# Optimization experiments

Measured on AMD Instinct MI355X. Metric: run time of the kernel, lower is better.

Reference implementation:

```python
import jax, jax.numpy as jnp
import numpy as np

N, C, HR, WR, HS, WS, S = 4, 128, 64, 64, 64, 64, 64


def setup_inputs() -> dict:
    key = jax.random.key(0)
    k1, k2, k3 = jax.random.split(key, 3)
    feat_ref = jax.random.normal(k1, (N, C, HR, WR), dtype=jnp.float32)
    feat_src = jax.random.normal(k2, (N, C, HS, WS), dtype=jnp.float32)
    # sampling locations in unnormalized source-pixel coordinates [0, WS)
    grids = jax.random.uniform(k3, (N, S, 2, HR, WR), dtype=jnp.float32) * WS
    mask = jnp.ones((N, S, HR, WR), dtype=jnp.float32)
    return {"feat_ref": feat_ref, "feat_src": feat_src, "grids": grids, "mask": mask}


def _corr_forward(feat_ref, feat_src, grids, mask):
    n, c, hr, wr = feat_ref.shape
    hs, ws = feat_src.shape[-2:]
    s = grids.shape[1]
    p = hr * wr
    fr = feat_ref.reshape(n, c, p)          # [N,C,P]
    fs = feat_src.reshape(n, c, hs * ws)    # [N,C,HsWs]
    # full pairwise correlation volume (normalize=False path)
    corr = jnp.einsum('ncp,ncq->npq', fr, fs)  # [N,P,HsWs]

    # grids NS2HrWr -> [N,P,2,S]  (matches permute(0,3,4,2,1).reshape)
    g = jnp.transpose(grids, (0, 3, 4, 2, 1)).reshape(n, p, 2, s)
    gx, gy = g[:, :, 0, :], g[:, :, 1, :]   # [N,P,S]

    # torch grid_sample, align_corners=False: normalized->pixel maps to coord-0.5
    ix = gx - 0.5
    iy = gy - 0.5
    x0 = jnp.floor(ix)
    y0 = jnp.floor(iy)
    wx1 = ix - x0
    wy1 = iy - y0
    x0i = x0.astype(jnp.int32)
    y0i = y0.astype(jnp.int32)

    out = jnp.zeros((n, p, s), corr.dtype)
    msum = jnp.zeros((n, p, s), corr.dtype)  # grid_sample of all-ones (zeros padding)
    for dx, wx in ((0, 1.0 - wx1), (1, wx1)):
        for dy, wy in ((0, 1.0 - wy1), (1, wy1)):
            xi = x0i + dx
            yi = y0i + dy
            inb = ((xi >= 0) & (xi < ws) & (yi >= 0) & (yi < hs)).astype(corr.dtype)
            idx = jnp.clip(yi, 0, hs - 1) * ws + jnp.clip(xi, 0, ws - 1)  # [N,P,S]
            val = jnp.take_along_axis(corr, idx, axis=-1)
            w = wx * wy * inb
            out = out + w * val
            msum = msum + w

    # mask[mask < 0.9999] = 0; mask[mask > 0] = 1
    corr_mask = jnp.where(msum < 0.9999, 0.0, 1.0).astype(corr.dtype)
    out = out * corr_mask

    # [N,P,S] -> [N,S,Hr,Wr]
    out = out.reshape(n, hr, wr, s).transpose(0, 3, 1, 2)
    corr_mask = corr_mask.reshape(n, hr, wr, s).transpose(0, 3, 1, 2)

    out = out * mask
    corr_mask = corr_mask * mask
    return out, corr_mask


def reference(feat_ref, feat_src, grids, mask):
    return _corr_forward(feat_ref, feat_src, grids, mask)
```

## Files before the change

kernel.cpp:

```cpp
#include <hip/hip_runtime.h>
#include <hip/hip_fp16.h>
#include <cstdint>
#include <cstddef>

#define NB 4
#define C 128
#define P 4096
#define S 64
#define Q 4096
#define WS_DIM 64
#define HS_DIM 64

#define FS_T_OFF 0

__device__ __forceinline__ void gload_lds16(const void* g, void* l) {
  __builtin_amdgcn_global_load_lds(
      (const __attribute__((address_space(1))) unsigned int*)g,
      (__attribute__((address_space(3))) unsigned int*)l, 16, 0, 0);
}

__global__ __launch_bounds__(256) void transpose_fs_h(
    const float* __restrict__ fs, __half* __restrict__ ws) {
  __shared__ float tile[32][65];
  int b = blockIdx.x;
  int n  = b >> 8;
  int t  = b & 255;
  int rti = t & 3;
  int cti = t >> 2;
  int r0 = rti << 5, c0 = cti << 6;
  const float* Sp = fs + (size_t)n * C * P;
  __half*      Dp = ws + FS_T_OFF + (size_t)n * Q * C;
  int tx = threadIdx.x & 15, ty = threadIdx.x >> 4;
#pragma unroll
  for (int i = 0; i < 2; ++i) {
    int row = ty + 16 * i;
    float4 v = *reinterpret_cast<const float4*>(
        &Sp[(size_t)(r0 + row) * P + c0 + tx * 4]);
    tile[row][tx * 4 + 0] = v.x;
    tile[row][tx * 4 + 1] = v.y;
    tile[row][tx * 4 + 2] = v.z;
    tile[row][tx * 4 + 3] = v.w;
  }
  __syncthreads();
  int ox = threadIdx.x & 7, oy = threadIdx.x >> 3;
#pragma unroll
  for (int i = 0; i < 2; ++i) {
    int prow = oy + 32 * i;
    __half2 h01 = __floats2half2_rn(tile[ox * 4 + 0][prow], tile[ox * 4 + 1][prow]);
    __half2 h23 = __floats2half2_rn(tile[ox * 4 + 2][prow], tile[ox * 4 + 3][prow]);
    uint2 pk;
    pk.x = *reinterpret_cast<unsigned int*>(&h01);
    pk.y = *reinterpret_cast<unsigned int*>(&h23);
    *reinterpret_cast<uint2*>(&Dp[(size_t)(c0 + prow) * C + r0 + ox * 4]) = pk;
  }
}

__global__ __launch_bounds__(256) void corr_main(
    const __half* __restrict__ ws, const float* __restrict__ fr_g,
    const float* __restrict__ grids, const float* __restrict__ mask,
    float* __restrict__ out, float* __restrict__ cmo) {
  const __half* fs_h = ws + FS_T_OFF;

  __shared__ __align__(16) unsigned char stg[4][16384];
  __shared__ int4   s_idx[4][65];
  __shared__ float4 s_w[4][65];
  __shared__ float  s_cmm[4][68];
  __shared__ float  s_out[4][68];
  __shared__ float  fr_lds[4][132];

  int b    = blockIdx.x;
  int xcd  = b & 7;
  int n    = xcd >> 1;
  int half = xcd & 1;
  int grp  = b >> 3;
  int wv   = threadIdx.x >> 6;
  int lane = threadIdx.x & 63;
  int t    = threadIdx.x;
  int p_base = ((half << 9) + grp) << 2;

#pragma unroll
  for (int i = 0; i < 2; ++i) {
    int e  = t + 256 * i;
    int c  = e >> 2;
    int po = e & 3;
    fr_lds[po][c] = fr_g[((size_t)n * C + c) * P + p_base + po];
  }

  {
    int s  = t >> 2;
    int po = t & 3;
    int pp = p_base + po;
    float gx = grids[(((size_t)n * S + s) * 2 + 0) * P + pp];
    float gy = grids[(((size_t)n * S + s) * 2 + 1) * P + pp];
    float mval = mask[((size_t)n * S + s) * P + pp];
    float ix = gx - 0.5f, iy = gy - 0.5f;
    float x0f = floorf(ix), y0f = floorf(iy);
    float wx1 = ix - x0f, wy1 = iy - y0f;
    float wx0 = 1.0f - wx1, wy0 = 1.0f - wy1;
    int x0 = (int)x0f, y0 = (int)y0f;
    int4 idx; float4 w4;
    float msum = 0.0f;
    {
      int xi = x0, yi = y0;
      bool inb = (xi >= 0) & (xi < WS_DIM) & (yi >= 0) & (yi < HS_DIM);
      float wk = inb ? wx0 * wy0 : 0.0f;
      msum += wk;
      idx.x = min(max(yi, 0), HS_DIM - 1) * WS_DIM + min(max(xi, 0), WS_DIM - 1);
      w4.x = wk;
    }
    {
      int xi = x0, yi = y0 + 1;
      bool inb = (xi >= 0) & (xi < WS_DIM) & (yi >= 0) & (yi < HS_DIM);
      float wk = inb ? wx0 * wy1 : 0.0f;
      msum += wk;
      idx.y = min(max(yi, 0), HS_DIM - 1) * WS_DIM + min(max(xi, 0), WS_DIM - 1);
      w4.y = wk;
    }
    {
      int xi = x0 + 1, yi = y0;
      bool inb = (xi >= 0) & (xi < WS_DIM) & (yi >= 0) & (yi < HS_DIM);
      float wk = inb ? wx1 * wy0 : 0.0f;
      msum += wk;
      idx.z = min(max(yi, 0), HS_DIM - 1) * WS_DIM + min(max(xi, 0), WS_DIM - 1);
      w4.z = wk;
    }
    {
      int xi = x0 + 1, yi = y0 + 1;
      bool inb = (xi >= 0) & (xi < WS_DIM) & (yi >= 0) & (yi < HS_DIM);
      float wk = inb ? wx1 * wy1 : 0.0f;
      msum += wk;
      idx.w = min(max(yi, 0), HS_DIM - 1) * WS_DIM + min(max(xi, 0), WS_DIM - 1);
      w4.w = wk;
    }
    float cm  = (msum < 0.9999f) ? 0.0f : 1.0f;
    float cmm = cm * mval;
    s_idx[po][s] = idx;
    s_w[po][s]   = w4;
    s_cmm[po][s] = cmm;
    cmo[((size_t)n * S + s) * P + pp] = cmm;
  }
  __syncthreads();

  int cg = lane & 3;
  int sl = lane >> 2;
  float frv[4][8];
#pragma unroll
  for (int j = 0; j < 4; ++j) {
    float4 a = *reinterpret_cast<const float4*>(&fr_lds[wv][j * 32 + cg * 8]);
    float4 bq = *reinterpret_cast<const float4*>(&fr_lds[wv][j * 32 + cg * 8 + 4]);
    frv[j][0] = a.x; frv[j][1] = a.y; frv[j][2] = a.z; frv[j][3] = a.w;
    frv[j][4] = bq.x; frv[j][5] = bq.y; frv[j][6] = bq.z; frv[j][7] = bq.w;
  }
  const __half* fsb = fs_h + (size_t)n * Q * C + cg * 8;
  unsigned char* mystg = &stg[wv][0];

#pragma unroll 1
  for (int r = 0; r < 4; ++r) {
    int s = r * 16 + sl;
    int4   id4 = s_idx[wv][s];
    float4 w4  = s_w[wv][s];
    float  cms = s_cmm[wv][s];
    const __half* q0 = fsb + (size_t)id4.x * C;
    const __half* q1 = fsb + (size_t)id4.y * C;
    const __half* q2 = fsb + (size_t)id4.z * C;
    const __half* q3 = fsb + (size_t)id4.w * C;

    __builtin_amdgcn_sched_barrier(0);
#pragma unroll
    for (int j = 0; j < 4; ++j) gload_lds16(q0 + j * 32, mystg + (0 * 4 + j) * 1024);
#pragma unroll
    for (int j = 0; j < 4; ++j) gload_lds16(q1 + j * 32, mystg + (1 * 4 + j) * 1024);
#pragma unroll
    for (int j = 0; j < 4; ++j) gload_lds16(q2 + j * 32, mystg + (2 * 4 + j) * 1024);
#pragma unroll
    for (int j = 0; j < 4; ++j) gload_lds16(q3 + j * 32, mystg + (3 * 4 + j) * 1024);

    float d0 = 0.0f, d1 = 0.0f, d2 = 0.0f, d3 = 0.0f;
    asm volatile("s_waitcnt vmcnt(8)" ::: "memory");
#pragma unroll
    for (int j = 0; j < 4; ++j) {
      const __half2* h0 = reinterpret_cast<const __half2*>(mystg + (0 * 4 + j) * 1024 + lane * 16);
      const __half2* h1 = reinterpret_cast<const __half2*>(mystg + (1 * 4 + j) * 1024 + lane * 16);
#pragma unroll
      for (int i = 0; i < 4; ++i) {
        float2 f0 = __half22float2(h0[i]);
        float2 f1 = __half22float2(h1[i]);
        d0 = fmaf(frv[j][2 * i], f0.x, d0);
        d0 = fmaf(frv[j][2 * i + 1], f0.y, d0);
        d1 = fmaf(frv[j][2 * i], f1.x, d1);
        d1 = fmaf(frv[j][2 * i + 1], f1.y, d1);
      }
    }
    asm volatile("s_waitcnt vmcnt(0)" ::: "memory");
#pragma unroll
    for (int j = 0; j < 4; ++j) {
      const __half2* h2 = reinterpret_cast<const __half2*>(mystg + (2 * 4 + j) * 1024 + lane * 16);
      const __half2* h3 = reinterpret_cast<const __half2*>(mystg + (3 * 4 + j) * 1024 + lane * 16);
#pragma unroll
      for (int i = 0; i < 4; ++i) {
        float2 f2 = __half22float2(h2[i]);
        float2 f3 = __half22float2(h3[i]);
        d2 = fmaf(frv[j][2 * i], f2.x, d2);
        d2 = fmaf(frv[j][2 * i + 1], f2.y, d2);
        d3 = fmaf(frv[j][2 * i], f3.x, d3);
        d3 = fmaf(frv[j][2 * i + 1], f3.y, d3);
      }
    }
    float acc = fmaf(w4.x, d0, 0.0f);
    acc = fmaf(w4.y, d1, acc);
    acc = fmaf(w4.z, d2, acc);
    acc = fmaf(w4.w, d3, acc);
    acc += __shfl_xor(acc, 1);
    acc += __shfl_xor(acc, 2);
    if (cg == 0) s_out[wv][s] = acc * cms;
  }
  __syncthreads();
  {
    int s = t >> 2, w2 = t & 3;
    out[((size_t)n * S + s) * P + (p_base + w2)] = s_out[w2][s];
  }
}

extern "C" void kernel_launch(void* const* d_in, const int* in_sizes, int n_in,
                              void* d_out, int out_size, void* d_ws, size_t ws_size,
                              hipStream_t stream) {
  const float* feat_ref = (const float*)d_in[0];
  const float* feat_src = (const float*)d_in[1];
  const float* grids    = (const float*)d_in[2];
  const float* mask     = (const float*)d_in[3];
  __half* ws = (__half*)d_ws;
  float* out = (float*)d_out;
  float* cmo = out + (size_t)NB * S * P;

  transpose_fs_h<<<1024, 256, 0, stream>>>(feat_src, ws);
  corr_main<<<4096, 256, 0, stream>>>(ws, feat_ref, grids, mask, out, cmo);
}
```

Measured before the change: 132.7 us.

## Fetch horizontally adjacent bilinear taps as one contiguous padded row span

Result: slower. 140.4 us (+5.8%).

```diff
diff --git a/kernel.cpp b/kernel.cpp
--- a/kernel.cpp
+++ b/kernel.cpp
@@ -11,7 +11,8 @@
 #define WS_DIM 64
 #define HS_DIM 64
 
-#define FS_T_OFF 0
+#define PADR  80
+#define NROWS 4256
 
 __device__ __forceinline__ void gload_lds16(const void* g, void* l) {
   __builtin_amdgcn_global_load_lds(
@@ -29,7 +30,7 @@
   int cti = t >> 2;
   int r0 = rti << 5, c0 = cti << 6;
   const float* Sp = fs + (size_t)n * C * P;
-  __half*      Dp = ws + FS_T_OFF + (size_t)n * Q * C;
+  __half*      Dp = ws + (size_t)n * NROWS * C + (size_t)PADR * C;
   int tx = threadIdx.x & 15, ty = threadIdx.x >> 4;
 #pragma unroll
   for (int i = 0; i < 2; ++i) {
@@ -59,10 +60,8 @@
     const __half* __restrict__ ws, const float* __restrict__ fr_g,
     const float* __restrict__ grids, const float* __restrict__ mask,
     float* __restrict__ out, float* __restrict__ cmo) {
-  const __half* fs_h = ws + FS_T_OFF;
-
   __shared__ __align__(16) unsigned char stg[4][16384];
-  __shared__ int4   s_idx[4][65];
+  __shared__ int    s_qb[4][68];
   __shared__ float4 s_w[4][65];
   __shared__ float  s_cmm[4][68];
   __shared__ float  s_out[4][68];
@@ -98,121 +97,99 @@
     float wx1 = ix - x0f, wy1 = iy - y0f;
     float wx0 = 1.0f - wx1, wy0 = 1.0f - wy1;
     int x0 = (int)x0f, y0 = (int)y0f;
-    int4 idx; float4 w4;
-    float msum = 0.0f;
-    {
-      int xi = x0, yi = y0;
-      bool inb = (xi >= 0) & (xi < WS_DIM) & (yi >= 0) & (yi < HS_DIM);
-      float wk = inb ? wx0 * wy0 : 0.0f;
-      msum += wk;
-      idx.x = min(max(yi, 0), HS_DIM - 1) * WS_DIM + min(max(xi, 0), WS_DIM - 1);
-      w4.x = wk;
-    }
-    {
-      int xi = x0, yi = y0 + 1;
-      bool inb = (xi >= 0) & (xi < WS_DIM) & (yi >= 0) & (yi < HS_DIM);
-      float wk = inb ? wx0 * wy1 : 0.0f;
-      msum += wk;
-      idx.y = min(max(yi, 0), HS_DIM - 1) * WS_DIM + min(max(xi, 0), WS_DIM - 1);
-      w4.y = wk;
-    }
-    {
-      int xi = x0 + 1, yi = y0;
-      bool inb = (xi >= 0) & (xi < WS_DIM) & (yi >= 0) & (yi < HS_DIM);
-      float wk = inb ? wx1 * wy0 : 0.0f;
-      msum += wk;
-      idx.z = min(max(yi, 0), HS_DIM - 1) * WS_DIM + min(max(xi, 0), WS_DIM - 1);
-      w4.z = wk;
-    }
-    {
-      int xi = x0 + 1, yi = y0 + 1;
-      bool inb = (xi >= 0) & (xi < WS_DIM) & (yi >= 0) & (yi < HS_DIM);
-      float wk = inb ? wx1 * wy1 : 0.0f;
-      msum += wk;
-      idx.w = min(max(yi, 0), HS_DIM - 1) * WS_DIM + min(max(xi, 0), WS_DIM - 1);
-      w4.w = wk;
-    }
+    bool bx0 = (x0 >= 0) & (x0 < WS_DIM);
+    bool bx1 = (x0 >= -1) & (x0 < WS_DIM - 1);
+    bool by0 = (y0 >= 0) & (y0 < HS_DIM);
+    bool by1 = (y0 >= -1) & (y0 < HS_DIM - 1);
+    float w00 = (bx0 & by0) ? wx0 * wy0 : 0.0f;
+    float w01 = (bx0 & by1) ? wx0 * wy1 : 0.0f;
+    float w10 = (bx1 & by0) ? wx1 * wy0 : 0.0f;
+    float w11 = (bx1 & by1) ? wx1 * wy1 : 0.0f;
+    float msum = ((w00 + w01) + w10) + w11;
     float cm  = (msum < 0.9999f) ? 0.0f : 1.0f;
     float cmm = cm * mval;
-    s_idx[po][s] = idx;
-    s_w[po][s]   = w4;
+    int qb = y0 * WS_DIM + x0;
+    qb = max(-PADR, min(qb, 4110));
+    s_qb[po][s]  = qb;
+    s_w[po][s]   = make_float4(w00, w10, w01, w11);
     s_cmm[po][s] = cmm;
     cmo[((size_t)n * S + s) * P + pp] = cmm;
   }
   __syncthreads();
 
-  int cg = lane & 3;
-  int sl = lane >> 2;
-  float frv[4][8];
-#pragma unroll
-  for (int j = 0; j < 4; ++j) {
-    float4 a = *reinterpret_cast<const float4*>(&fr_lds[wv][j * 32 + cg * 8]);
-    float4 bq = *reinterpret_cast<const float4*>(&fr_lds[wv][j * 32 + cg * 8 + 4]);
-    frv[j][0] = a.x; frv[j][1] = a.y; frv[j][2] = a.z; frv[j][3] = a.w;
-    frv[j][4] = bq.x; frv[j][5] = bq.y; frv[j][6] = bq.z; frv[j][7] = bq.w;
-  }
-  const __half* fsb = fs_h + (size_t)n * Q * C + cg * 8;
+  int o  = lane & 7;
+  int sl = lane >> 3;
+  float fr0[8], fr1[8];
+  {
+    float4 a = *reinterpret_cast<const float4*>(&fr_lds[wv][o * 8]);
+    float4 bq = *reinterpret_cast<const float4*>(&fr_lds[wv][o * 8 + 4]);
+    fr0[0] = a.x; fr0[1] = a.y; fr0[2] = a.z; fr0[3] = a.w;
+    fr0[4] = bq.x; fr0[5] = bq.y; fr0[6] = bq.z; fr0[7] = bq.w;
+    float4 c = *reinterpret_cast<const float4*>(&fr_lds[wv][64 + o * 8]);
+    float4 d = *reinterpret_cast<const float4*>(&fr_lds[wv][64 + o * 8 + 4]);
+    fr1[0] = c.x; fr1[1] = c.y; fr1[2] = c.z; fr1[3] = c.w;
+    fr1[4] = d.x; fr1[5] = d.y; fr1[6] = d.z; fr1[7] = d.w;
+  }
+  const __half* fsn = ws + (size_t)n * NROWS * C + (size_t)PADR * C;
   unsigned char* mystg = &stg[wv][0];
 
 #pragma unroll 1
   for (int r = 0; r < 4; ++r) {
-    int s = r * 16 + sl;
-    int4   id4 = s_idx[wv][s];
-    float4 w4  = s_w[wv][s];
-    float  cms = s_cmm[wv][s];
-    const __half* q0 = fsb + (size_t)id4.x * C;
-    const __half* q1 = fsb + (size_t)id4.y * C;
-    const __half* q2 = fsb + (size_t)id4.z * C;
-    const __half* q3 = fsb + (size_t)id4.w * C;
-
     __builtin_amdgcn_sched_barrier(0);
 #pragma unroll
-    for (int j = 0; j < 4; ++j) gload_lds16(q0 + j * 32, mystg + (0 * 4 + j) * 1024);
-#pragma unroll
-    for (int j = 0; j < 4; ++j) gload_lds16(q1 + j * 32, mystg + (1 * 4 + j) * 1024);
-#pragma unroll
-    for (int j = 0; j < 4; ++j) gload_lds16(q2 + j * 32, mystg + (2 * 4 + j) * 1024);
-#pragma unroll
-    for (int j = 0; j < 4; ++j) gload_lds16(q3 + j * 32, mystg + (3 * 4 + j) * 1024);
-
-    float d0 = 0.0f, d1 = 0.0f, d2 = 0.0f, d3 = 0.0f;
-    asm volatile("s_waitcnt vmcnt(8)" ::: "memory");
-#pragma unroll
-    for (int j = 0; j < 4; ++j) {
-      const __half2* h0 = reinterpret_cast<const __half2*>(mystg + (0 * 4 + j) * 1024 + lane * 16);
-      const __half2* h1 = reinterpret_cast<const __half2*>(mystg + (1 * 4 + j) * 1024 + lane * 16);
-#pragma unroll
-      for (int i = 0; i < 4; ++i) {
-        float2 f0 = __half22float2(h0[i]);
-        float2 f1 = __half22float2(h1[i]);
-        d0 = fmaf(frv[j][2 * i], f0.x, d0);
-        d0 = fmaf(frv[j][2 * i + 1], f0.y, d0);
-        d1 = fmaf(frv[j][2 * i], f1.x, d1);
-        d1 = fmaf(frv[j][2 * i + 1], f1.y, d1);
+    for (int h = 0; h < 2; ++h) {
+      int s = r * 16 + h * 8 + sl;
+      int qb = s_qb[wv][s];
+#pragma unroll
+      for (int y = 0; y < 2; ++y) {
+        const __half* src = fsn + (long)(qb + y * 64) * C + o * 8;
+#pragma unroll
+        for (int j = 0; j < 4; ++j)
+          gload_lds16(src + j * 64, mystg + ((h * 2 + y) * 4 + j) * 1024);
       }
     }
-    asm volatile("s_waitcnt vmcnt(0)" ::: "memory");
-#pragma unroll
-    for (int j = 0; j < 4; ++j) {
-      const __half2* h2 = reinterpret_cast<const __half2*>(mystg + (2 * 4 + j) * 1024 + lane * 16);
-      const __half2* h3 = reinterpret_cast<const __half2*>(mystg + (3 * 4 + j) * 1024 + lane * 16);
-#pragma unroll
-      for (int i = 0; i < 4; ++i) {
-        float2 f2 = __half22float2(h2[i]);
-        float2 f3 = __half22float2(h3[i]);
-        d2 = fmaf(frv[j][2 * i], f2.x, d2);
-        d2 = fmaf(frv[j][2 * i + 1], f2.y, d2);
-        d3 = fmaf(frv[j][2 * i], f3.x, d3);
-        d3 = fmaf(frv[j][2 * i + 1], f3.y, d3);
+
+#pragma unroll
+    for (int h = 0; h < 2; ++h) {
+      if (h == 0) { asm volatile("s_waitcnt vmcnt(8)" ::: "memory"); }
+      else        { asm volatile("s_waitcnt vmcnt(0)" ::: "memory"); }
+      int s = r * 16 + h * 8 + sl;
+      float4 w4  = s_w[wv][s];
+      float  cms = s_cmm[wv][s];
+      float acc = 0.0f;
+#pragma unroll
+      for (int y = 0; y < 2; ++y) {
+        const unsigned char* base = mystg + ((h * 2 + y) * 4) * 1024 + lane * 16;
+        const __half2* b0 = reinterpret_cast<const __half2*>(base);
+        const __half2* b1 = reinterpret_cast<const __half2*>(base + 1024);
+        const __half2* b2 = reinterpret_cast<const __half2*>(base + 2048);
+        const __half2* b3 = reinterpret_cast<const __half2*>(base + 3072);
+        float d0 = 0.0f, d1 = 0.0f;
+#pragma unroll
+        for (int i = 0; i < 4; ++i) {
+          float2 f0 = __half22float2(b0[i]);
+          float2 f1 = __half22float2(b1[i]);
+          float2 f2 = __half22float2(b2[i]);
+          float2 f3 = __half22float2(b3[i]);
+          d0 = fmaf(fr0[2 * i], f0.x, d0);
+          d0 = fmaf(fr0[2 * i + 1], f0.y, d0);
+          d0 = fmaf(fr1[2 * i], f1.x, d0);
+          d0 = fmaf(fr1[2 * i + 1], f1.y, d0);
+          d1 = fmaf(fr0[2 * i], f2.x, d1);
+          d1 = fmaf(fr0[2 * i + 1], f2.y, d1);
+          d1 = fmaf(fr1[2 * i], f3.x, d1);
+          d1 = fmaf(fr1[2 * i + 1], f3.y, d1);
+        }
+        float wA = (y == 0) ? w4.x : w4.z;
+        float wB = (y == 0) ? w4.y : w4.w;
+        acc = fmaf(wA, d0, acc);
+        acc = fmaf(wB, d1, acc);
       }
+      acc += __shfl_xor(acc, 1);
+      acc += __shfl_xor(acc, 2);
+      acc += __shfl_xor(acc, 4);
+      if (o == 0) s_out[wv][s] = acc * cms;
     }
-    float acc = fmaf(w4.x, d0, 0.0f);
-    acc = fmaf(w4.y, d1, acc);
-    acc = fmaf(w4.z, d2, acc);
-    acc = fmaf(w4.w, d3, acc);
-    acc += __shfl_xor(acc, 1);
-    acc += __shfl_xor(acc, 2);
-    if (cg == 0) s_out[wv][s] = acc * cms;
   }
   __syncthreads();
   {
```
